# Kernel tuning notes

Hardware: AMD Instinct MI355X
Metric: run time of the kernel (lower is better)

## Reference

```python
import jax, jax.numpy as jnp
import numpy as np
from jax import lax

B, N, C_IN = 8, 16384, 32
NPOINT = 1024
RADII = (0.5, 1.0)
NSAMPLES = (16, 32)
MLPS = ((35, 32, 64), (35, 64, 128))  # first dim includes +3 for use_xyz


def setup_inputs():
    key = jax.random.key(0)
    ks = jax.random.split(key, 20)
    inp = {
        'xyz': jax.random.normal(ks[0], (B, N, 3), jnp.float32),
        'features': jax.random.normal(ks[1], (B, C_IN, N), jnp.float32),
    }
    i = 2
    for bi, spec in enumerate(MLPS):
        for li in range(len(spec) - 1):
            cin, cout = spec[li], spec[li + 1]
            inp['w%d_%d' % (bi, li)] = jax.random.normal(ks[i], (cout, cin), jnp.float32) * np.float32(1.0 / np.sqrt(cin)); i += 1
            inp['s%d_%d' % (bi, li)] = jax.random.uniform(ks[i], (cout,), jnp.float32, minval=0.5, maxval=1.5); i += 1
            inp['b%d_%d' % (bi, li)] = jax.random.normal(ks[i], (cout,), jnp.float32) * 0.1; i += 1
    return inp


def _fps(xyz, npoint):
    # iterative D-FPS, start from index 0 (matches CUDA furthest_point_sampling)
    Bb, Nn, _ = xyz.shape
    def body(carry, _):
        dists, far = carry
        centroid = jnp.take_along_axis(xyz, far[:, None, None], axis=1)  # (B,1,3)
        d = jnp.sum((xyz - centroid) ** 2, axis=-1)                       # (B,N)
        dists = jnp.minimum(dists, d)
        return (dists, jnp.argmax(dists, axis=-1).astype(jnp.int32)), far
    init = (jnp.full((Bb, Nn), 1e10, jnp.float32), jnp.zeros((Bb,), jnp.int32))
    _, idx = lax.scan(body, init, None, length=npoint)
    return idx.T  # (B, npoint)


def _ball_query(dist2, radius, nsample):
    # first-nsample-in-index-order semantics of pointnet2 ball_query;
    # empty slots padded with first hit (0 if no hit at all)
    Nn = dist2.shape[-1]
    scores = jnp.where(dist2 < radius * radius, jnp.arange(Nn, dtype=jnp.int32), Nn)
    neg, _ = lax.top_k(-scores, nsample)  # nsample smallest indices
    idx = -neg
    first = jnp.where(idx[..., :1] == Nn, 0, idx[..., :1])
    return jnp.where(idx == Nn, first, idx)


def _forward(xyz, features, params):
    fwx = jnp.concatenate([xyz.transpose(0, 2, 1), features], axis=1)   # (B,3+C,N)
    fps_idx = _fps(xyz, NPOINT)                                          # (B,P) int32
    new_xyz = jnp.take_along_axis(xyz, fps_idx[:, :, None], axis=1)      # (B,P,3)
    # pairwise squared distances via gemm (B,P,N)
    xx = jnp.sum(xyz * xyz, axis=-1)
    qq = jnp.sum(new_xyz * new_xyz, axis=-1)
    dist2 = qq[:, :, None] + xx[:, None, :] - 2.0 * jnp.einsum('bpd,bnd->bpn', new_xyz, xyz)
    centers = new_xyz.transpose(0, 2, 1)[..., None]                      # (B,3,P,1)
    outs = []
    for k in range(len(RADII)):
        idx = _ball_query(dist2, RADII[k], NSAMPLES[k])                  # (B,P,S)
        grouped = jax.vmap(lambda f, i: f[:, i])(fwx, idx)               # (B,3+C,P,S)
        x = jnp.concatenate([grouped[:, :3] - centers, grouped[:, 3:]], axis=1)
        for (w, s, b) in params[k]:
            # 1x1 Conv2d (no bias) + eval-mode BN folded into (s,b) + ReLU
            x = jax.nn.relu(jnp.einsum('oc,bcps->bops', w, x) * s[None, :, None, None] + b[None, :, None, None])
        outs.append(jnp.max(x, axis=-1))                                 # max_pool over nsample
    return new_xyz, jnp.concatenate(outs, axis=1)                        # (B,P,3), (B,192,P)


def reference(xyz, features, w0_0, s0_0, b0_0, w0_1, s0_1, b0_1, w1_0, s1_0, b1_0, w1_1, s1_1, b1_1):
    params = [[(w0_0, s0_0, b0_0), (w0_1, s0_1, b0_1)],
              [(w1_0, s1_0, b1_0), (w1_1, s1_1, b1_1)]]
    return _forward(xyz, features, params)
```

## Files before the change

kernel.cpp:

```cpp
#include <hip/hip_runtime.h>

#define B 8
#define N 16384
#define C_IN 32
#define P 1024

#define R16(OP) OP(0) OP(1) OP(2) OP(3) OP(4) OP(5) OP(6) OP(7) \
                OP(8) OP(9) OP(10) OP(11) OP(12) OP(13) OP(14) OP(15)
#define G0(OP) OP(0) OP(1) OP(2) OP(3)
#define G1(OP) OP(4) OP(5) OP(6) OP(7)
#define G2(OP) OP(8) OP(9) OP(10) OP(11)
#define G3(OP) OP(12) OP(13) OP(14) OP(15)

template <int CTRL>
__device__ __forceinline__ float dpp_fmax(float v) {
  float o = __int_as_float(__builtin_amdgcn_update_dpp(
      __float_as_int(v), __float_as_int(v), CTRL, 0xF, 0xF, false));
  return fmaxf(v, o);
}

__global__ __launch_bounds__(1024)
void fps_kernel(const float* __restrict__ xyz, float* __restrict__ new_xyz)
{
  __shared__ float2 sxy[N];
  __shared__ unsigned long long slot[2];

  const int b = blockIdx.x;
  const int t = threadIdx.x;
  const float* xb = xyz + (size_t)b * (N * 3);

  if (t == 0) { slot[0] = ~0ull; slot[1] = ~0ull; }

#define FPS_DECL(i) float pz##i, dm##i = 1e10f;
  R16(FPS_DECL)
#define FPS_LOAD(i) { const int n = t + (i << 10);                             \
    float x = xb[n * 3 + 0];                                                   \
    float y = xb[n * 3 + 1];                                                   \
    pz##i   = xb[n * 3 + 2];                                                   \
    asm volatile("" : "+v"(pz##i));     \
    sxy[n] = make_float2(x, y); }
  R16(FPS_LOAD)

  const int bpa16 = ((t & 63) ^ 16) << 2;
  const int bpa32 = ((t & 63) ^ 32) << 2;

  float cz = xb[2];
  __syncthreads();
  float2 c0 = sxy[0];
  float cx = c0.x, cy = c0.y;
  float mx = 0.f, my = 0.f, mz = 0.f;

  for (int iter = 0; iter < P; ++iter) {
    bool keep = (t == iter);
    mx = keep ? cx : mx;
    my = keep ? cy : my;
    mz = keep ? cz : mz;
    if (iter == P - 1) break;

    float bestv = -1.0f;
    int   bi = 0;
#define FPS_PRE(i) float2 q##i = sxy[t + (i << 10)];
#define FPS_CALC(i) {                                                          \
    float dx = __fsub_rn(q##i.x, cx);                                          \
    float dy = __fsub_rn(q##i.y, cy);                                          \
    float dz = __fsub_rn(pz##i, cz);                                           \
    float d  = __fadd_rn(__fadd_rn(__fmul_rn(dx, dx), __fmul_rn(dy, dy)),      \
                         __fmul_rn(dz, dz));                                   \
    dm##i = fminf(dm##i, d);                                                   \
    bool better = dm##i > bestv;                                               \
    bestv = better ? dm##i : bestv;                                            \
    bi    = better ? i      : bi; }
    { G0(FPS_PRE) G0(FPS_CALC) }
    { G1(FPS_PRE) G1(FPS_CALC) }
    { G2(FPS_PRE) G2(FPS_CALC) }
    { G3(FPS_PRE) G3(FPS_CALC) }

    float wm = bestv;
    wm = dpp_fmax<0xB1>(wm);
    wm = dpp_fmax<0x4E>(wm);
    wm = dpp_fmax<0x141>(wm);
    wm = dpp_fmax<0x140>(wm);
    wm = fmaxf(wm, __int_as_float(
        __builtin_amdgcn_ds_bpermute(bpa16, __float_as_int(wm))));
    wm = fmaxf(wm, __int_as_float(
        __builtin_amdgcn_ds_bpermute(bpa32, __float_as_int(wm))));

    if (bestv == wm) {
      unsigned nn  = (unsigned)(t + (bi << 10));
      unsigned inv = ~__float_as_uint(bestv);
      unsigned long long key =
          ((unsigned long long)(unsigned)(P - 1 - iter) << 46) |
          ((unsigned long long)inv << 14) |
          (unsigned long long)nn;
      atomicMin(&slot[iter & 1], key);
    }
    __syncthreads();

    unsigned long long k = slot[iter & 1];
    int sel = __builtin_amdgcn_readfirstlane((int)((unsigned)k & 0x3FFFu));
    float2 nxy = sxy[sel];
    cx = nxy.x;
    cy = nxy.y;
    cz = xb[sel * 3 + 2];
  }

  {
    size_t o = ((size_t)b * P + t) * 3;
    new_xyz[o + 0] = mx;
    new_xyz[o + 1] = my;
    new_xyz[o + 2] = mz;
  }
#undef FPS_DECL
#undef FPS_LOAD
#undef FPS_PRE
#undef FPS_CALC
}

__global__ __launch_bounds__(256) void ballq_kernel(
    const float* __restrict__ xyz, const float* __restrict__ new_xyz,
    int* __restrict__ idx0, int* __restrict__ idx1)
{
  const int wid  = blockIdx.x * 4 + (threadIdx.x >> 6);
  const int lane = threadIdx.x & 63;
  const int b = wid >> 10;
  const int p = wid & (P - 1);
  const float* xb = xyz + (size_t)b * (N * 3);
  const size_t bp = (size_t)b * P + p;
  const float cx = new_xyz[bp * 3 + 0];
  const float cy = new_xyz[bp * 3 + 1];
  const float cz = new_xyz[bp * 3 + 2];
  const float qv = __fadd_rn(__fadd_rn(__fmul_rn(cx, cx), __fmul_rn(cy, cy)),
                             __fmul_rn(cz, cz));
  int* __restrict__ o0 = idx0 + bp * 16;
  int* __restrict__ o1 = idx1 + bp * 32;

  int c0 = 0, c1 = 0, f0 = 0, f1 = 0;
  const unsigned long long below = (1ull << lane) - 1ull;

  for (int base = 0; base < N; base += 64) {
    int n = base + lane;
    float x = xb[n * 3 + 0], y = xb[n * 3 + 1], z = xb[n * 3 + 2];
    float xxv = __fadd_rn(__fadd_rn(__fmul_rn(x, x), __fmul_rn(y, y)),
                          __fmul_rn(z, z));
    float dot = __fadd_rn(__fadd_rn(__fmul_rn(cx, x), __fmul_rn(cy, y)),
                          __fmul_rn(cz, z));
    float d2 = __fsub_rn(__fadd_rn(qv, xxv), __fmul_rn(2.0f, dot));
    unsigned long long m0 = __ballot(d2 < 0.25f);
    unsigned long long m1 = __ballot(d2 < 1.0f);
    if (c0 == 0 && m0) f0 = base + __builtin_ctzll(m0);
    if (c1 == 0 && m1) f1 = base + __builtin_ctzll(m1);
    if ((m0 >> lane) & 1ull) {
      int pos = c0 + (int)__builtin_popcountll(m0 & below);
      if (pos < 16) o0[pos] = n;
    }
    if ((m1 >> lane) & 1ull) {
      int pos = c1 + (int)__builtin_popcountll(m1 & below);
      if (pos < 32) o1[pos] = n;
    }
    c0 = min(16, c0 + (int)__builtin_popcountll(m0));
    c1 = min(32, c1 + (int)__builtin_popcountll(m1));
    if (c0 >= 16 && c1 >= 32) break;
  }
  for (int s = c0 + lane; s < 16; s += 64) o0[s] = f0;
  for (int s = c1 + lane; s < 32; s += 64) o1[s] = f1;
}

template <int S, int C1, int C2, int CH_OFF>
__global__ __launch_bounds__(256) void mlp_kernel(
    const float* __restrict__ xyz, const float* __restrict__ feats,
    const float* __restrict__ new_xyz, const int* __restrict__ idx,
    const float* __restrict__ w1, const float* __restrict__ s1,
    const float* __restrict__ b1, const float* __restrict__ w2,
    const float* __restrict__ s2, const float* __restrict__ b2,
    float* __restrict__ out)
{
  static_assert((C1 * S) % 256 == 0 && (C2 * S) % 256 == 0, "mapping");
  __shared__ float wl1[35][C1];
  __shared__ float wl2[C1][C2];
  __shared__ float sb1[2][C1];
  __shared__ float sb2[2][C2];
  __shared__ float xs[35][S];
  __shared__ float o1s[C1][S];
  __shared__ float pm[256];

  const int tid = threadIdx.x;
  for (int i = tid; i < 35 * C1; i += 256) {
    int o = i % C1, c = i / C1;
    wl1[c][o] = w1[o * 35 + c];
  }
  for (int i = tid; i < C1 * C2; i += 256) {
    int o = i % C2, c = i / C2;
    wl2[c][o] = w2[o * C1 + c];
  }
  if (tid < C1) { sb1[0][tid] = s1[tid]; sb1[1][tid] = b1[tid]; }
  if (tid < C2) { sb2[0][tid] = s2[tid]; sb2[1][tid] = b2[tid]; }

  const int b  = blockIdx.x / (P / 8);
  const int p0 = (blockIdx.x % (P / 8)) * 8;
  const float* xb = xyz + (size_t)b * (N * 3);
  const float* fb = feats + (size_t)b * (C_IN * N);
  __syncthreads();

  for (int pi = 0; pi < 8; ++pi) {
    const int p = p0 + pi;
    const size_t bp = (size_t)b * P + p;
    const int* ip = idx + bp * S;
    const float cx = new_xyz[bp * 3 + 0];
    const float cy = new_xyz[bp * 3 + 1];
    const float cz = new_xyz[bp * 3 + 2];
    for (int i = tid; i < 35 * S; i += 256) {
      int c = i / S, s = i % S;
      int n = ip[s];
      float v;
      if (c == 0)      v = xb[n * 3 + 0] - cx;
      else if (c == 1) v = xb[n * 3 + 1] - cy;
      else if (c == 2) v = xb[n * 3 + 2] - cz;
      else             v = fb[(size_t)(c - 3) * N + n];
      xs[c][s] = v;
    }
    __syncthreads();
    {
      constexpr int OPT = (C1 * S) / 256;
      const int s  = tid % S;
      const int ob = (tid / S) * OPT;
      float acc[OPT];
#pragma unroll
      for (int j = 0; j < OPT; ++j) acc[j] = 0.0f;
      for (int c = 0; c < 35; ++c) {
        float xv = xs[c][s];
#pragma unroll
        for (int j = 0; j < OPT; ++j) acc[j] = fmaf(xv, wl1[c][ob + j], acc[j]);
      }
#pragma unroll
      for (int j = 0; j < OPT; ++j) {
        float v = fmaf(acc[j], sb1[0][ob + j], sb1[1][ob + j]);
        o1s[ob + j][s] = fmaxf(v, 0.0f);
      }
    }
    __syncthreads();
    {
      constexpr int NS = (C2 * S) / 256;
      const int o2 = tid % C2;
      const int sb = (tid / C2) * NS;
      float acc[NS];
#pragma unroll
      for (int j = 0; j < NS; ++j) acc[j] = 0.0f;
      for (int c = 0; c < C1; ++c) {
        float wv = wl2[c][o2];
#pragma unroll
        for (int j = 0; j < NS; ++j) acc[j] = fmaf(wv, o1s[c][sb + j], acc[j]);
      }
      const float scale = sb2[0][o2], bias = sb2[1][o2];
      float m = 0.0f;
#pragma unroll
      for (int j = 0; j < NS; ++j) {
        float v = fmaf(acc[j], scale, bias);
        m = fmaxf(m, v);
      }
      pm[tid] = m;
      __syncthreads();
      if (tid < C2) {
        float mm = pm[tid];
#pragma unroll
        for (int g = 1; g < 256 / C2; ++g) mm = fmaxf(mm, pm[tid + g * C2]);
        out[((size_t)b * 192 + CH_OFF + tid) * P + p] = mm;
      }
    }
    __syncthreads();
  }
}

extern "C" void kernel_launch(void* const* d_in, const int* in_sizes, int n_in,
                              void* d_out, int out_size, void* d_ws, size_t ws_size,
                              hipStream_t stream) {
  const float* xyz   = (const float*)d_in[0];
  const float* feats = (const float*)d_in[1];
  const float* w0_0 = (const float*)d_in[2];
  const float* s0_0 = (const float*)d_in[3];
  const float* b0_0 = (const float*)d_in[4];
  const float* w0_1 = (const float*)d_in[5];
  const float* s0_1 = (const float*)d_in[6];
  const float* b0_1 = (const float*)d_in[7];
  const float* w1_0 = (const float*)d_in[8];
  const float* s1_0 = (const float*)d_in[9];
  const float* b1_0 = (const float*)d_in[10];
  const float* w1_1 = (const float*)d_in[11];
  const float* s1_1 = (const float*)d_in[12];
  const float* b1_1 = (const float*)d_in[13];

  float* out      = (float*)d_out;
  float* new_xyz  = out;
  float* feat_out = out + (size_t)B * P * 3;

  char* w = (char*)d_ws;
  int* idx0 = (int*)w; w += (size_t)B * P * 16 * sizeof(int);
  int* idx1 = (int*)w; w += (size_t)B * P * 32 * sizeof(int);

  fps_kernel<<<dim3(B), dim3(1024), 0, stream>>>(xyz, new_xyz);
  ballq_kernel<<<dim3(B * P / 4), dim3(256), 0, stream>>>(xyz, new_xyz, idx0, idx1);
  mlp_kernel<16, 32, 64, 0><<<dim3(B * P / 8), dim3(256), 0, stream>>>(
      xyz, feats, new_xyz, idx0, w0_0, s0_0, b0_0, w0_1, s0_1, b0_1, feat_out);
  mlp_kernel<32, 64, 128, 64><<<dim3(B * P / 8), dim3(256), 0, stream>>>(
      xyz, feats, new_xyz, idx1, w1_0, s1_0, b1_0, w1_1, s1_1, b1_1, feat_out);
}
```

Measured before the change: 2.303 ms.

## Vectorize FPS inner loop with packed FP32 math and SoA shared layout

Reworks the furthest-point-sampling kernel so shared memory holds x and y in separate arrays, and each thread owns 4 contiguous points per group, loaded with float4 LDS reads. Distance computation uses v_pk_add/v_pk_mul packed FP32 instructions on pairs of points, with negated centroids so subtraction becomes packed add. The output now stores the selected index and re-reads coordinates at the end instead of keeping them in registers. This cuts VALU and LDS instruction count in the serial 1024-iteration loop, at the cost of different point-to-thread mapping and register pairing.

```diff
diff --git a/kernel.cpp b/kernel.cpp
--- a/kernel.cpp
+++ b/kernel.cpp
@@ -5,12 +5,20 @@
 #define C_IN 32
 #define P 1024
 
-#define R16(OP) OP(0) OP(1) OP(2) OP(3) OP(4) OP(5) OP(6) OP(7) \
-                OP(8) OP(9) OP(10) OP(11) OP(12) OP(13) OP(14) OP(15)
-#define G0(OP) OP(0) OP(1) OP(2) OP(3)
-#define G1(OP) OP(4) OP(5) OP(6) OP(7)
-#define G2(OP) OP(8) OP(9) OP(10) OP(11)
-#define G3(OP) OP(12) OP(13) OP(14) OP(15)
+typedef float v2f __attribute__((ext_vector_type(2)));
+typedef unsigned long long ull;
+
+#define R8(OP) OP(0) OP(1) OP(2) OP(3) OP(4) OP(5) OP(6) OP(7)
+
+__device__ __forceinline__ v2f pk_add(v2f a, v2f b) {
+  v2f d; asm("v_pk_add_f32 %0, %1, %2" : "=v"(d) : "v"(a), "v"(b)); return d;
+}
+__device__ __forceinline__ v2f pk_mul(v2f a, v2f b) {
+  v2f d; asm("v_pk_mul_f32 %0, %1, %2" : "=v"(d) : "v"(a), "v"(b)); return d;
+}
+__device__ __forceinline__ float negf(float x) {
+  return __int_as_float(__float_as_int(x) ^ 0x80000000);
+}
 
 template <int CTRL>
 __device__ __forceinline__ float dpp_fmax(float v) {
@@ -22,8 +30,9 @@
 __global__ __launch_bounds__(1024)
 void fps_kernel(const float* __restrict__ xyz, float* __restrict__ new_xyz)
 {
-  __shared__ float2 sxy[N];
-  __shared__ unsigned long long slot[2];
+  __shared__ __align__(16) float sx[N];
+  __shared__ __align__(16) float sy[N];
+  __shared__ ull slot[2];
 
   const int b = blockIdx.x;
   const int t = threadIdx.x;
@@ -31,49 +40,63 @@
 
   if (t == 0) { slot[0] = ~0ull; slot[1] = ~0ull; }
 
-#define FPS_DECL(i) float pz##i, dm##i = 1e10f;
-  R16(FPS_DECL)
-#define FPS_LOAD(i) { const int n = t + (i << 10);                             \
-    float x = xb[n * 3 + 0];                                                   \
-    float y = xb[n * 3 + 1];                                                   \
-    pz##i   = xb[n * 3 + 2];                                                   \
-    asm volatile("" : "+v"(pz##i));     \
-    sxy[n] = make_float2(x, y); }
-  R16(FPS_LOAD)
+#define FPS_DECL(j) v2f pzp##j, dmp##j; dmp##j.x = 1e10f; dmp##j.y = 1e10f;
+  R8(FPS_DECL)
+#define FPS_LOADP(j) {                                                         \
+    const int n0 = (t << 2) + ((j >> 1) << 12) + ((j & 1) << 1);               \
+    const float2 ld0 = *(const float2*)&xb[(size_t)n0 * 3 + 0];     \
+    const float2 ld1 = *(const float2*)&xb[(size_t)n0 * 3 + 2];     \
+    const float2 ld2 = *(const float2*)&xb[(size_t)n0 * 3 + 4];     \
+    sx[n0]     = ld0.x;  sy[n0]     = ld0.y;                                   \
+    sx[n0 + 1] = ld1.y;  sy[n0 + 1] = ld2.x;                                   \
+    pzp##j.x   = ld1.x;  pzp##j.y   = ld2.y;                                   \
+    asm volatile("" : "+v"(pzp##j)); }
+  R8(FPS_LOADP)
 
   const int bpa16 = ((t & 63) ^ 16) << 2;
   const int bpa32 = ((t & 63) ^ 32) << 2;
 
   float cz = xb[2];
   __syncthreads();
-  float2 c0 = sxy[0];
-  float cx = c0.x, cy = c0.y;
-  float mx = 0.f, my = 0.f, mz = 0.f;
+  float cx = sx[0], cy = sy[0];
+  int sel = 0, msel = 0;
 
   for (int iter = 0; iter < P; ++iter) {
-    bool keep = (t == iter);
-    mx = keep ? cx : mx;
-    my = keep ? cy : my;
-    mz = keep ? cz : mz;
+    msel = (t == iter) ? sel : msel;
     if (iter == P - 1) break;
 
+    v2f cxx, cyy, czz;
+    { float v = negf(cx); cxx.x = v; cxx.y = v; }
+    { float v = negf(cy); cyy.x = v; cyy.y = v; }
+    { float v = negf(cz); czz.x = v; czz.y = v; }
+
     float bestv = -1.0f;
-    int   bi = 0;
-#define FPS_PRE(i) float2 q##i = sxy[t + (i << 10)];
-#define FPS_CALC(i) {                                                          \
-    float dx = __fsub_rn(q##i.x, cx);                                          \
-    float dy = __fsub_rn(q##i.y, cy);                                          \
-    float dz = __fsub_rn(pz##i, cz);                                           \
-    float d  = __fadd_rn(__fadd_rn(__fmul_rn(dx, dx), __fmul_rn(dy, dy)),      \
-                         __fmul_rn(dz, dz));                                   \
-    dm##i = fminf(dm##i, d);                                                   \
-    bool better = dm##i > bestv;                                               \
-    bestv = better ? dm##i : bestv;                                            \
-    bi    = better ? i      : bi; }
-    { G0(FPS_PRE) G0(FPS_CALC) }
-    { G1(FPS_PRE) G1(FPS_CALC) }
-    { G2(FPS_PRE) G2(FPS_CALC) }
-    { G3(FPS_PRE) G3(FPS_CALC) }
+    int   s = 0;
+
+#define FPS_PAIR(xa, ya, j, s0, s1) {                                          \
+      v2f dx = pk_add(xa, cxx), dy = pk_add(ya, cyy);                          \
+      v2f sq = pk_add(pk_mul(dx, dx), pk_mul(dy, dy));                         \
+      v2f dz = pk_add(pzp##j, czz);                                            \
+      v2f dd = pk_add(sq, pk_mul(dz, dz));                                     \
+      dmp##j.x = fminf(dmp##j.x, dd.x);                                        \
+      dmp##j.y = fminf(dmp##j.y, dd.y);                                        \
+      bool b0 = dmp##j.x > bestv;                                              \
+      bestv = b0 ? dmp##j.x : bestv;  s = b0 ? (s0) : s;                       \
+      bool b1 = dmp##j.y > bestv;                                              \
+      bestv = b1 ? dmp##j.y : bestv;  s = b1 ? (s1) : s; }
+
+#define FPS_GROUP(i, ja, jb) {                                                 \
+      const float4 qx = *(const float4*)&sx[(t << 2) + ((i) << 12)];           \
+      const float4 qy = *(const float4*)&sy[(t << 2) + ((i) << 12)];           \
+      v2f xl; xl.x = qx.x; xl.y = qx.y;  v2f yl; yl.x = qy.x; yl.y = qy.y;     \
+      v2f xh; xh.x = qx.z; xh.y = qx.w;  v2f yh; yh.x = qy.z; yh.y = qy.w;     \
+      FPS_PAIR(xl, yl, ja, 2 * (ja), 2 * (ja) + 1)                             \
+      FPS_PAIR(xh, yh, jb, 2 * (jb), 2 * (jb) + 1) }
+
+    FPS_GROUP(0, 0, 1)
+    FPS_GROUP(1, 2, 3)
+    FPS_GROUP(2, 4, 5)
+    FPS_GROUP(3, 6, 7)
 
     float wm = bestv;
     wm = dpp_fmax<0xB1>(wm);
@@ -86,34 +109,32 @@
         __builtin_amdgcn_ds_bpermute(bpa32, __float_as_int(wm))));
 
     if (bestv == wm) {
-      unsigned nn  = (unsigned)(t + (bi << 10));
+      int nn = (t << 2) + ((s & 12) << 10) + (s & 3);
       unsigned inv = ~__float_as_uint(bestv);
-      unsigned long long key =
-          ((unsigned long long)(unsigned)(P - 1 - iter) << 46) |
-          ((unsigned long long)inv << 14) |
-          (unsigned long long)nn;
+      ull key = ((ull)(unsigned)(P - 1 - iter) << 46) |
+                ((ull)inv << 14) | (ull)(unsigned)nn;
       atomicMin(&slot[iter & 1], key);
     }
     __syncthreads();
 
-    unsigned long long k = slot[iter & 1];
-    int sel = __builtin_amdgcn_readfirstlane((int)((unsigned)k & 0x3FFFu));
-    float2 nxy = sxy[sel];
-    cx = nxy.x;
-    cy = nxy.y;
-    cz = xb[sel * 3 + 2];
+    ull k = slot[iter & 1];
+    sel = __builtin_amdgcn_readfirstlane((int)((unsigned)k & 0x3FFFu));
+    cx = sx[sel];
+    cy = sy[sel];
+    cz = xb[(size_t)sel * 3 + 2];
   }
 
   {
+    const int n = msel;
     size_t o = ((size_t)b * P + t) * 3;
-    new_xyz[o + 0] = mx;
-    new_xyz[o + 1] = my;
-    new_xyz[o + 2] = mz;
+    new_xyz[o + 0] = sx[n];
+    new_xyz[o + 1] = sy[n];
+    new_xyz[o + 2] = xb[(size_t)n * 3 + 2];
   }
 #undef FPS_DECL
-#undef FPS_LOAD
-#undef FPS_PRE
-#undef FPS_CALC
+#undef FPS_LOADP
+#undef FPS_PAIR
+#undef FPS_GROUP
 }
 
 __global__ __launch_bounds__(256) void ballq_kernel(
```

New measurement: 2.305 ms. Within noise of the previous version (+0.1%).
